# Kernel optimization log

Hardware: AMD Instinct MI355X
Metric: run time of the kernel (lower is better)

The kernel has to match this reference:

```python
import jax, jax.numpy as jnp
import numpy as np

K = 1.0            # curvature (manifold.k); sqrt(K)=1 simplifies formulas
EPS = 1e-5         # module eps used in variance rescale
MIN_NORM = 1e-8    # clamp for sqrt of Lorentz inners
MAX_EUCLID = 10.0  # rescale_to_max_euclid cap (keeps cosh/sinh in fp32 range)


def l_inner(x, y):
    # Lorentz inner product <x,y>_L = -x0*y0 + <x_s, y_s>, keepdim
    return -x[..., :1] * y[..., :1] + jnp.sum(x[..., 1:] * y[..., 1:], axis=-1, keepdims=True)


def centroid(x):
    # Lorentzian centroid over the group axis (dim=-2)
    avg = jnp.mean(x, axis=-2, keepdims=True)
    denom = jnp.sqrt(jnp.clip(-l_inner(avg, avg), MIN_NORM, None))
    return avg / denom


def logmap(x, y):
    alpha = jnp.clip(-l_inner(x, y), 1.0 + 1e-7, None)   # -<x,y>_L >= 1
    dist = jnp.arccosh(alpha)
    nomin = y - alpha * x                                # y + <x,y>_L * x
    denom = jnp.sqrt(jnp.clip(l_inner(nomin, nomin), MIN_NORM, None))
    return dist * nomin / denom


def _plus_origin(p):
    # p + o where o = (1, 0, ..., 0)
    return jnp.concatenate([p[..., :1] + 1.0, p[..., 1:]], axis=-1)


def transp0back(x, v):
    # parallel transport of tangent v at x back to the origin o
    nom = -v[..., :1]                 # <o, v>_L = -v0
    denom = 1.0 + x[..., :1]          # K - <x, o>_L = 1 + x0
    return v + (nom / denom) * _plus_origin(x)


def transp0(y, v):
    # parallel transport of tangent v at origin o to point y
    nom = l_inner(y, v)
    denom = 1.0 + y[..., :1]          # K - <o, y>_L = 1 + y0
    return v + (nom / denom) * _plus_origin(y)


def rescale_to_max_euclid(u):
    n = jnp.linalg.norm(u, axis=-1, keepdims=True)
    scale = jnp.minimum(1.0, MAX_EUCLID / jnp.clip(n, MIN_NORM, None))
    return u * scale


def expmap(x, u):
    nrm = jnp.sqrt(jnp.clip(l_inner(u, u), MIN_NORM, None))
    return jnp.cosh(nrm) * x + jnp.sinh(nrm) * (u / nrm)


def setup_inputs() -> dict:
    key = jax.random.key(0)
    k1, = jax.random.split(key, 1)
    bs, h, w, c = 64, 56, 56, 128
    # sample spatial components, lift onto the hyperboloid: x0 = sqrt(1+|xs|^2)
    xs = 0.5 * jax.random.normal(k1, (bs, h, w, c - 1), dtype=jnp.float32)
    x0 = jnp.sqrt(1.0 + jnp.sum(xs * xs, axis=-1, keepdims=True))
    x = jnp.concatenate([x0, xs], axis=-1)
    gamma = jnp.ones((c,), dtype=jnp.float32)
    # beta = manifold.origin(c) = (1, 0, ..., 0)
    beta = jnp.zeros((c,), dtype=jnp.float32).at[0].set(1.0)
    return {"x": x, "gamma": gamma, "beta": beta, "groups": 8}


def reference(x, gamma, beta, groups):
    bs, h, w, c = x.shape
    xg = x.reshape(bs, -1, groups, c)                    # (bs, hw/g, g, c)
    mean = centroid(xg)                                  # (bs, hw/g, 1, c)
    x_T = logmap(mean, xg)                               # tangent at mean
    x_T = transp0back(mean, x_T)                         # tangent at origin
    # Frechet-style variance: mean Euclidean norm over spatial dim (dim=1)
    var = jnp.mean(jnp.linalg.norm(x_T, axis=-1, keepdims=True), axis=1, keepdims=True)
    x_T = x_T * (gamma / (var + EPS))
    x_T = rescale_to_max_euclid(x_T)
    x_T = transp0(beta, x_T)                             # transport to beta
    out = expmap(beta, x_T)
    return out.reshape(bs, h, w, c)
```

## Files before the change

### kernel.cpp

```cpp
#include <hip/hip_runtime.h>
#include <math.h>


constexpr int S_GROUPS = 392;
constexpr int N_GROUPS = 64 * S_GROUPS;
constexpr int CSTRIDE = 160;

__device__ __forceinline__ void wave_lds_fence() {
  __asm__ volatile("" ::: "memory");
  __builtin_amdgcn_wave_barrier();
  __asm__ volatile("" ::: "memory");
}

__device__ __forceinline__ void rsum8x3(float& a, float& b, float& c) {
#pragma unroll
  for (int m = 1; m <= 4; m <<= 1) {
    a += __shfl_xor(a, m, 64);
    b += __shfl_xor(b, m, 64);
    c += __shfl_xor(c, m, 64);
  }
}

__device__ __forceinline__ void fold_mean(const float v[16], int lane,
                                          float& c0, float& c1) {
  float a8[8];
  const bool h5 = (lane & 32) != 0;
#pragma unroll
  for (int i = 0; i < 8; ++i) {
    float kp = h5 ? v[i + 8] : v[i];
    float sd = h5 ? v[i] : v[i + 8];
    a8[i] = kp + __shfl_xor(sd, 32, 64);
  }
  float a4[4];
  const bool h4 = (lane & 16) != 0;
#pragma unroll
  for (int i = 0; i < 4; ++i) {
    float kp = h4 ? a8[i + 4] : a8[i];
    float sd = h4 ? a8[i] : a8[i + 4];
    a4[i] = kp + __shfl_xor(sd, 16, 64);
  }
  const bool h3 = (lane & 8) != 0;
  float kp0 = h3 ? a4[2] : a4[0], sd0 = h3 ? a4[0] : a4[2];
  float kp1 = h3 ? a4[3] : a4[1], sd1 = h3 ? a4[1] : a4[3];
  c0 = (kp0 + __shfl_xor(sd0, 8, 64)) * 0.125f;
  c1 = (kp1 + __shfl_xor(sd1, 8, 64)) * 0.125f;
}

struct CoreOut {
  float avg[16];
  float sc, k, coef;
  float iaL, dpL, yyE, y0p, avg0;
};

__device__ __forceinline__ void core(const float v[16], int lane,
                                     float* __restrict__ smrow,
                                     float* __restrict__ gc, CoreOut& o) {
  const int p = lane >> 3, q = lane & 7;
  float c0, c1;
  fold_mean(v, lane, c0, c1);
  *reinterpret_cast<float2*>(&smrow[q * 16 + p * 2]) = make_float2(c0, c1);
  *reinterpret_cast<float2*>(&gc[q * 16 + p * 2]) = make_float2(c0, c1);
  wave_lds_fence();
#pragma unroll
  for (int j = 0; j < 4; ++j)
    *reinterpret_cast<float4*>(&o.avg[4 * j]) =
        *reinterpret_cast<const float4*>(&smrow[q * 16 + 4 * j]);
  wave_lds_fence();

  float pa = 0.f, pd = 0.f, py = 0.f;
#pragma unroll
  for (int i = 0; i < 16; ++i) {
    pa = fmaf(o.avg[i], o.avg[i], pa);
    pd = fmaf(o.avg[i], v[i], pd);
    py = fmaf(v[i], v[i], py);
  }
  if (q == 0) {
    pa -= 2.f * o.avg[0] * o.avg[0];
    pd -= 2.f * o.avg[0] * v[0];
  }
  rsum8x3(pa, pd, py);
  o.iaL = pa;
  o.dpL = pd;
  o.yyE = py;
  o.y0p = __shfl(v[0], lane & 56, 64);
  o.avg0 = __shfl(o.avg[0], 0, 64);

  float rden = rsqrtf(fmaxf(-pa, 1e-8f));
  float a_raw = -pd * rden;
  float alpha = fmaxf(a_raw, 1.f + 1e-7f);
  float t = alpha - 1.f;
  float dist = log1pf(t + sqrtf(t * (alpha + 1.f)));
  float yyL = py - 2.f * o.y0p * o.y0p;
  float inn = fmaxf(yyL + 2.f * alpha * a_raw - alpha * alpha, 1e-8f);
  o.sc = dist * rsqrtf(inn);
  float am = alpha * rden;
  float mean0 = rden * o.avg0;
  float v0 = o.sc * (o.y0p - am * o.avg0);
  o.coef = -v0 / (1.f + mean0);
  o.k = o.coef * rden - o.sc * am;

  if (q == 0)
    *reinterpret_cast<float4*>(&gc[128 + p * 4]) =
        make_float4(o.sc, o.k, o.coef, 0.f);
}

__device__ __forceinline__ float xt_norm(const CoreOut& A) {
  float yavgE = A.dpL + 2.f * A.avg0 * A.y0p;
  float aaE = A.iaL + 2.f * A.avg0 * A.avg0;
  float nsq = A.sc * A.sc * A.yyE + A.k * A.k * aaE + 2.f * A.sc * A.k * yavgE +
              A.coef * A.coef + 2.f * A.coef * (A.sc * A.y0p + A.k * A.avg0);
  return sqrtf(fmaxf(nsq, 0.f));
}

__global__ __launch_bounds__(256) void lngn_pass1(const float* __restrict__ x,
                                                  float* __restrict__ var_part,
                                                  float* __restrict__ cache) {
  __shared__ float sm[4][2][128];
  const int w = threadIdx.x >> 6, lane = threadIdx.x & 63;
  const int p = lane >> 3, q = lane & 7;
  const int wid0 = (blockIdx.x * 4 + w) * 2;
  const float* b0 = x + (size_t)wid0 * 1024 + p * 128 + q * 16;
  float vA[16], vB[16];
#pragma unroll
  for (int j = 0; j < 4; ++j) {
    *reinterpret_cast<float4*>(&vA[4 * j]) =
        *reinterpret_cast<const float4*>(b0 + 4 * j);
    *reinterpret_cast<float4*>(&vB[4 * j]) =
        *reinterpret_cast<const float4*>(b0 + 1024 + 4 * j);
  }
  CoreOut A, B;
  core(vA, lane, sm[w][0], cache + (size_t)wid0 * CSTRIDE, A);
  core(vB, lane, sm[w][1], cache + (size_t)(wid0 + 1) * CSTRIDE, B);
  float nA = xt_norm(A), nB = xt_norm(B);
  if (q == 0) {
    const int b = wid0 / S_GROUPS;
    const int s = wid0 - b * S_GROUPS;
    var_part[(size_t)(b * 8 + p) * S_GROUPS + s] = nA;
    var_part[(size_t)(b * 8 + p) * S_GROUPS + s + 1] = nB;
  }
}

__global__ __launch_bounds__(256) void lngn_finalize(
    const float* __restrict__ var_part, float* __restrict__ var_out) {
  const int wv = (int)((blockIdx.x * 256 + threadIdx.x) >> 6);
  const int lane = threadIdx.x & 63;
  const float* base = var_part + (size_t)wv * S_GROUPS;
  float s = 0.f;
  for (int s0 = lane; s0 < S_GROUPS; s0 += 64) s += base[s0];
#pragma unroll
  for (int m = 32; m >= 1; m >>= 1) s += __shfl_xor(s, m, 64);
  if (lane == 0) var_out[wv] = s * (1.f / (float)S_GROUPS);
}

__global__ __launch_bounds__(256) void lngn_pass2(
    const float* __restrict__ x, const float* __restrict__ gamma,
    const float* __restrict__ beta, const float* __restrict__ var,
    const float* __restrict__ cache, float* __restrict__ out) {
  const int w = threadIdx.x >> 6, lane = threadIdx.x & 63;
  const int p = lane >> 3, q = lane & 7;
  const int wid = blockIdx.x * 4 + w;
  const size_t base = (size_t)wid * 1024 + p * 128 + q * 16;
  const float* gc = cache + (size_t)wid * CSTRIDE;

  float v[16], av[16], gm[16], bt[16];
#pragma unroll
  for (int j = 0; j < 4; ++j) {
    *reinterpret_cast<float4*>(&v[4 * j]) =
        *reinterpret_cast<const float4*>(x + base + 4 * j);
    *reinterpret_cast<float4*>(&av[4 * j]) =
        *reinterpret_cast<const float4*>(gc + q * 16 + 4 * j);
    *reinterpret_cast<float4*>(&gm[4 * j]) =
        *reinterpret_cast<const float4*>(gamma + q * 16 + 4 * j);
    *reinterpret_cast<float4*>(&bt[4 * j]) =
        *reinterpret_cast<const float4*>(beta + q * 16 + 4 * j);
  }
  const float4 sk = *reinterpret_cast<const float4*>(gc + 128 + p * 4);
  const float sc = sk.x, kk = sk.y, coef = sk.z;

  const int b = wid / S_GROUPS;
  const float s1 = 1.f / (var[b * 8 + p] + 1e-5f);

  float u[16];
  float pe = 0.f, pb = 0.f, pbb = 0.f;
#pragma unroll
  for (int i = 0; i < 16; ++i) {
    float xt = fmaf(sc, v[i], kk * av[i]);
    if (i == 0) xt += (q == 0) ? coef : 0.f;
    u[i] = xt * (gm[i] * s1);
    pe = fmaf(u[i], u[i], pe);
    pb = fmaf(bt[i], u[i], pb);
    pbb = fmaf(bt[i], bt[i], pbb);
  }
  if (q == 0) {
    pb -= 2.f * bt[0] * u[0];
    pbb -= 2.f * bt[0] * bt[0];
  }
  rsum8x3(pe, pb, pbb);
  const float u0 = __shfl(u[0], 0, 64);
  const float bt0 = __shfl(bt[0], 0, 64);

  float n = sqrtf(pe);
  float scl = fminf(1.f, 10.f / fmaxf(n, 1e-8f));
  float c2 = scl * pb / (1.f + bt0);
  float uuL = pe - 2.f * u0 * u0;
  float innw = scl * scl * uuL + 2.f * scl * c2 * (pb - u0) +
               c2 * c2 * (pbb - 2.f * bt0 - 1.f);
  float nrm = sqrtf(fmaxf(innw, 1e-8f));
  float e = expf(nrm), ie = 1.f / e;
  float chv = 0.5f * (e + ie);
  float isn = (0.5f * (e - ie)) / nrm;
  float C1 = chv + isn * c2, C2 = isn * scl, C3 = isn * c2;
  float o16[16];
#pragma unroll
  for (int i = 0; i < 16; ++i) o16[i] = fmaf(C1, bt[i], C2 * u[i]);
  if (q == 0) o16[0] += C3;
  float* ob = out + base;
#pragma unroll
  for (int j = 0; j < 4; ++j)
    *reinterpret_cast<float4*>(ob + 4 * j) =
        *reinterpret_cast<const float4*>(&o16[4 * j]);
}

extern "C" void kernel_launch(void* const* d_in, const int* in_sizes, int n_in,
                              void* d_out, int out_size, void* d_ws,
                              size_t ws_size, hipStream_t stream) {
  const float* x = (const float*)d_in[0];
  const float* gamma = (const float*)d_in[1];
  const float* beta = (const float*)d_in[2];
  float* out = (float*)d_out;
  float* var_part = (float*)d_ws;
  float* var_final = var_part + (size_t)N_GROUPS * 8;
  float* cache = var_final + 512;

  lngn_pass1<<<N_GROUPS / 8, 256, 0, stream>>>(x, var_part, cache);
  lngn_finalize<<<128, 256, 0, stream>>>(var_part, var_final);
  lngn_pass2<<<N_GROUPS / 4, 256, 0, stream>>>(x, gamma, beta, var_final, cache,
                                               out);
}
```

Before: 232.5 us.

## Precompute per-group gamma-weighted reductions in pass1 to remove pass2 reductions

Result: faster. 208.6 us (-10.3%).

```diff
diff --git a/kernel.cpp b/kernel.cpp
--- a/kernel.cpp
+++ b/kernel.cpp
@@ -4,7 +4,7 @@
 
 constexpr int S_GROUPS = 392;
 constexpr int N_GROUPS = 64 * S_GROUPS;
-constexpr int CSTRIDE = 160;
+constexpr int CSTRIDE = 192;
 
 __device__ __forceinline__ void wave_lds_fence() {
   __asm__ volatile("" ::: "memory");
@@ -49,10 +49,11 @@
 struct CoreOut {
   float avg[16];
   float sc, k, coef;
-  float iaL, dpL, yyE, y0p, avg0;
+  float nvar;
 };
 
-__device__ __forceinline__ void core(const float v[16], int lane,
+__device__ __forceinline__ void core(const float v[16], const float gm[16],
+                                     const float bt[16], int lane,
                                      float* __restrict__ smrow,
                                      float* __restrict__ gc, CoreOut& o) {
   const int p = lane >> 3, q = lane & 7;
@@ -79,69 +80,80 @@
     pd -= 2.f * o.avg[0] * v[0];
   }
   rsum8x3(pa, pd, py);
-  o.iaL = pa;
-  o.dpL = pd;
-  o.yyE = py;
-  o.y0p = __shfl(v[0], lane & 56, 64);
-  o.avg0 = __shfl(o.avg[0], 0, 64);
+  const float y0p = __shfl(v[0], lane & 56, 64);
+  const float avg0 = __shfl(o.avg[0], 0, 64);
 
   float rden = rsqrtf(fmaxf(-pa, 1e-8f));
   float a_raw = -pd * rden;
   float alpha = fmaxf(a_raw, 1.f + 1e-7f);
   float t = alpha - 1.f;
   float dist = log1pf(t + sqrtf(t * (alpha + 1.f)));
-  float yyL = py - 2.f * o.y0p * o.y0p;
+  float yyL = py - 2.f * y0p * y0p;
   float inn = fmaxf(yyL + 2.f * alpha * a_raw - alpha * alpha, 1e-8f);
   o.sc = dist * rsqrtf(inn);
   float am = alpha * rden;
-  float mean0 = rden * o.avg0;
-  float v0 = o.sc * (o.y0p - am * o.avg0);
+  float mean0 = rden * avg0;
+  float v0 = o.sc * (y0p - am * avg0);
   o.coef = -v0 / (1.f + mean0);
   o.k = o.coef * rden - o.sc * am;
 
-  if (q == 0)
-    *reinterpret_cast<float4*>(&gc[128 + p * 4]) =
-        make_float4(o.sc, o.k, o.coef, 0.f);
-}
-
-__device__ __forceinline__ float xt_norm(const CoreOut& A) {
-  float yavgE = A.dpL + 2.f * A.avg0 * A.y0p;
-  float aaE = A.iaL + 2.f * A.avg0 * A.avg0;
-  float nsq = A.sc * A.sc * A.yyE + A.k * A.k * aaE + 2.f * A.sc * A.k * yavgE +
-              A.coef * A.coef + 2.f * A.coef * (A.sc * A.y0p + A.k * A.avg0);
-  return sqrtf(fmaxf(nsq, 0.f));
-}
-
-__global__ __launch_bounds__(256) void lngn_pass1(const float* __restrict__ x,
-                                                  float* __restrict__ var_part,
-                                                  float* __restrict__ cache) {
+  float na = 0.f, pe = 0.f, pb = 0.f, xt0 = 0.f, gx0 = 0.f;
+#pragma unroll
+  for (int i = 0; i < 16; ++i) {
+    float xt = fmaf(o.sc, v[i], o.k * o.avg[i]);
+    if (i == 0) xt += (q == 0) ? o.coef : 0.f;
+    float gx = gm[i] * xt;
+    na = fmaf(xt, xt, na);
+    pe = fmaf(gx, gx, pe);
+    pb = fmaf(bt[i], gx, pb);
+    if (i == 0) { xt0 = xt; gx0 = gx; }
+  }
+  if (q == 0) pb -= 2.f * bt[0] * gx0;
+  rsum8x3(na, pe, pb);
+  o.nvar = sqrtf(na);
+  if (q == 0) {
+    *reinterpret_cast<float4*>(&gc[128 + p * 8]) =
+        make_float4(o.sc, o.k, o.coef, pe);
+    *reinterpret_cast<float4*>(&gc[128 + p * 8 + 4]) =
+        make_float4(pb, xt0, 0.f, 0.f);
+  }
+}
+
+__global__ __launch_bounds__(256) void lngn_pass1(
+    const float* __restrict__ x, const float* __restrict__ gamma,
+    const float* __restrict__ beta, float* __restrict__ var_part,
+    float* __restrict__ cache) {
   __shared__ float sm[4][2][128];
   const int w = threadIdx.x >> 6, lane = threadIdx.x & 63;
   const int p = lane >> 3, q = lane & 7;
   const int wid0 = (blockIdx.x * 4 + w) * 2;
   const float* b0 = x + (size_t)wid0 * 1024 + p * 128 + q * 16;
-  float vA[16], vB[16];
+  float vA[16], vB[16], gm[16], bt[16];
 #pragma unroll
   for (int j = 0; j < 4; ++j) {
     *reinterpret_cast<float4*>(&vA[4 * j]) =
         *reinterpret_cast<const float4*>(b0 + 4 * j);
     *reinterpret_cast<float4*>(&vB[4 * j]) =
         *reinterpret_cast<const float4*>(b0 + 1024 + 4 * j);
+    *reinterpret_cast<float4*>(&gm[4 * j]) =
+        *reinterpret_cast<const float4*>(gamma + q * 16 + 4 * j);
+    *reinterpret_cast<float4*>(&bt[4 * j]) =
+        *reinterpret_cast<const float4*>(beta + q * 16 + 4 * j);
   }
   CoreOut A, B;
-  core(vA, lane, sm[w][0], cache + (size_t)wid0 * CSTRIDE, A);
-  core(vB, lane, sm[w][1], cache + (size_t)(wid0 + 1) * CSTRIDE, B);
-  float nA = xt_norm(A), nB = xt_norm(B);
+  core(vA, gm, bt, lane, sm[w][0], cache + (size_t)wid0 * CSTRIDE, A);
+  core(vB, gm, bt, lane, sm[w][1], cache + (size_t)(wid0 + 1) * CSTRIDE, B);
   if (q == 0) {
     const int b = wid0 / S_GROUPS;
     const int s = wid0 - b * S_GROUPS;
-    var_part[(size_t)(b * 8 + p) * S_GROUPS + s] = nA;
-    var_part[(size_t)(b * 8 + p) * S_GROUPS + s + 1] = nB;
+    var_part[(size_t)(b * 8 + p) * S_GROUPS + s] = A.nvar;
+    var_part[(size_t)(b * 8 + p) * S_GROUPS + s + 1] = B.nvar;
   }
 }
 
 __global__ __launch_bounds__(256) void lngn_finalize(
-    const float* __restrict__ var_part, float* __restrict__ var_out) {
+    const float* __restrict__ var_part, const float* __restrict__ beta,
+    float* __restrict__ var_out) {
   const int wv = (int)((blockIdx.x * 256 + threadIdx.x) >> 6);
   const int lane = threadIdx.x & 63;
   const float* base = var_part + (size_t)wv * S_GROUPS;
@@ -150,6 +162,16 @@
 #pragma unroll
   for (int m = 32; m >= 1; m >>= 1) s += __shfl_xor(s, m, 64);
   if (lane == 0) var_out[wv] = s * (1.f / (float)S_GROUPS);
+
+  if (blockIdx.x == 0 && threadIdx.x < 64) {
+    const int l = threadIdx.x;
+    float b0v = beta[2 * l], b1v = beta[2 * l + 1];
+    float tsum = b0v * b0v + b1v * b1v;
+    if (l == 0) tsum -= 2.f * b0v * b0v;
+#pragma unroll
+    for (int m = 32; m >= 1; m >>= 1) tsum += __shfl_xor(tsum, m, 64);
+    if (l == 0) var_out[512] = tsum;
+  }
 }
 
 __global__ __launch_bounds__(256) void lngn_pass2(
@@ -157,68 +179,66 @@
     const float* __restrict__ beta, const float* __restrict__ var,
     const float* __restrict__ cache, float* __restrict__ out) {
   const int w = threadIdx.x >> 6, lane = threadIdx.x & 63;
-  const int p = lane >> 3, q = lane & 7;
   const int wid = blockIdx.x * 4 + w;
-  const size_t base = (size_t)wid * 1024 + p * 128 + q * 16;
+  const float* xb = x + (size_t)wid * 1024;
   const float* gc = cache + (size_t)wid * CSTRIDE;
-
-  float v[16], av[16], gm[16], bt[16];
+  const int cl = lane & 31;
+  const int par = lane >> 5;
+
+  float4 xv[4];
+#pragma unroll
+  for (int j = 0; j < 4; ++j)
+    xv[j] = *reinterpret_cast<const float4*>(xb + j * 256 + 4 * lane);
+  const float4 av = *reinterpret_cast<const float4*>(gc + 4 * cl);
+  const float4 gm4 = *reinterpret_cast<const float4*>(gamma + 4 * cl);
+  const float4 bt4 = *reinterpret_cast<const float4*>(beta + 4 * cl);
+
+  const int pix = lane & 7;
+  const float4 s0 = *reinterpret_cast<const float4*>(gc + 128 + pix * 8);
+  const float4 s1v = *reinterpret_cast<const float4*>(gc + 128 + pix * 8 + 4);
+  const float sc = s0.x, kk = s0.y, coef = s0.z, PE = s0.w;
+  const float PB = s1v.x, XT0 = s1v.y;
+  const int b = wid / S_GROUPS;
+  const float varv = var[b * 8 + pix];
+  const float pbb = var[512];
+  const float bt0 = beta[0], gm0 = gamma[0];
+
+  const float is1 = 1.f / (varv + 1e-5f);
+  const float pe = is1 * is1 * PE;
+  const float pb = is1 * PB;
+  const float u0 = is1 * gm0 * XT0;
+  const float n = sqrtf(pe);
+  const float scl = fminf(1.f, 10.f / fmaxf(n, 1e-8f));
+  const float c2 = scl * pb / (1.f + bt0);
+  const float uuL = pe - 2.f * u0 * u0;
+  const float innw = scl * scl * uuL + 2.f * scl * c2 * (pb - u0) +
+                     c2 * c2 * (pbb - 2.f * bt0 - 1.f);
+  const float nrm = sqrtf(fmaxf(innw, 1e-8f));
+  const float e = expf(nrm), ie = 1.f / e;
+  const float chv = 0.5f * (e + ie);
+  const float isn = (0.5f * (e - ie)) / nrm;
+  const float A1 = chv + isn * c2;
+  const float Cu = isn * scl * is1;
+  const float A2 = Cu * sc;
+  const float A3 = Cu * kk;
+  const float A4 = fmaf(Cu * gm0, coef, isn * c2);
+
+  float* ob = out + (size_t)wid * 1024;
 #pragma unroll
   for (int j = 0; j < 4; ++j) {
-    *reinterpret_cast<float4*>(&v[4 * j]) =
-        *reinterpret_cast<const float4*>(x + base + 4 * j);
-    *reinterpret_cast<float4*>(&av[4 * j]) =
-        *reinterpret_cast<const float4*>(gc + q * 16 + 4 * j);
-    *reinterpret_cast<float4*>(&gm[4 * j]) =
-        *reinterpret_cast<const float4*>(gamma + q * 16 + 4 * j);
-    *reinterpret_cast<float4*>(&bt[4 * j]) =
-        *reinterpret_cast<const float4*>(beta + q * 16 + 4 * j);
-  }
-  const float4 sk = *reinterpret_cast<const float4*>(gc + 128 + p * 4);
-  const float sc = sk.x, kk = sk.y, coef = sk.z;
-
-  const int b = wid / S_GROUPS;
-  const float s1 = 1.f / (var[b * 8 + p] + 1e-5f);
-
-  float u[16];
-  float pe = 0.f, pb = 0.f, pbb = 0.f;
-#pragma unroll
-  for (int i = 0; i < 16; ++i) {
-    float xt = fmaf(sc, v[i], kk * av[i]);
-    if (i == 0) xt += (q == 0) ? coef : 0.f;
-    u[i] = xt * (gm[i] * s1);
-    pe = fmaf(u[i], u[i], pe);
-    pb = fmaf(bt[i], u[i], pb);
-    pbb = fmaf(bt[i], bt[i], pbb);
-  }
-  if (q == 0) {
-    pb -= 2.f * bt[0] * u[0];
-    pbb -= 2.f * bt[0] * bt[0];
-  }
-  rsum8x3(pe, pb, pbb);
-  const float u0 = __shfl(u[0], 0, 64);
-  const float bt0 = __shfl(bt[0], 0, 64);
-
-  float n = sqrtf(pe);
-  float scl = fminf(1.f, 10.f / fmaxf(n, 1e-8f));
-  float c2 = scl * pb / (1.f + bt0);
-  float uuL = pe - 2.f * u0 * u0;
-  float innw = scl * scl * uuL + 2.f * scl * c2 * (pb - u0) +
-               c2 * c2 * (pbb - 2.f * bt0 - 1.f);
-  float nrm = sqrtf(fmaxf(innw, 1e-8f));
-  float e = expf(nrm), ie = 1.f / e;
-  float chv = 0.5f * (e + ie);
-  float isn = (0.5f * (e - ie)) / nrm;
-  float C1 = chv + isn * c2, C2 = isn * scl, C3 = isn * c2;
-  float o16[16];
-#pragma unroll
-  for (int i = 0; i < 16; ++i) o16[i] = fmaf(C1, bt[i], C2 * u[i]);
-  if (q == 0) o16[0] += C3;
-  float* ob = out + base;
-#pragma unroll
-  for (int j = 0; j < 4; ++j)
-    *reinterpret_cast<float4*>(ob + 4 * j) =
-        *reinterpret_cast<const float4*>(&o16[4 * j]);
+    const int sp = 2 * j + par;
+    const float a1 = __shfl(A1, sp, 64);
+    const float a2 = __shfl(A2, sp, 64);
+    const float a3 = __shfl(A3, sp, 64);
+    const float a4 = __shfl(A4, sp, 64);
+    float4 o4;
+    o4.x = fmaf(a1, bt4.x, gm4.x * fmaf(a2, xv[j].x, a3 * av.x));
+    o4.y = fmaf(a1, bt4.y, gm4.y * fmaf(a2, xv[j].y, a3 * av.y));
+    o4.z = fmaf(a1, bt4.z, gm4.z * fmaf(a2, xv[j].z, a3 * av.z));
+    o4.w = fmaf(a1, bt4.w, gm4.w * fmaf(a2, xv[j].w, a3 * av.w));
+    if (cl == 0) o4.x += a4;
+    *reinterpret_cast<float4*>(ob + j * 256 + 4 * lane) = o4;
+  }
 }
 
 extern "C" void kernel_launch(void* const* d_in, const int* in_sizes, int n_in,
@@ -230,10 +250,10 @@
   float* out = (float*)d_out;
   float* var_part = (float*)d_ws;
   float* var_final = var_part + (size_t)N_GROUPS * 8;
-  float* cache = var_final + 512;
-
-  lngn_pass1<<<N_GROUPS / 8, 256, 0, stream>>>(x, var_part, cache);
-  lngn_finalize<<<128, 256, 0, stream>>>(var_part, var_final);
+  float* cache = var_part + 201472;
+
+  lngn_pass1<<<N_GROUPS / 8, 256, 0, stream>>>(x, gamma, beta, var_part, cache);
+  lngn_finalize<<<128, 256, 0, stream>>>(var_part, beta, var_final);
   lngn_pass2<<<N_GROUPS / 4, 256, 0, stream>>>(x, gamma, beta, var_final, cache,
                                                out);
 }
```
